# Optimization experiments

Measured on AMD Instinct MI355X. Metric: run time of the kernel, lower is better.

The kernel has to match this reference:

```python
import jax, jax.numpy as jnp
import numpy as np

B, M, H = 8, 2048, 1024


def setup_inputs() -> dict:
    key = jax.random.key(0)
    k0, k1, k2, k3, k4 = jax.random.split(key, 5)
    return {
        "query": jax.random.normal(k0, (B, M, H), dtype=jnp.float32),
        "key": jax.random.normal(k1, (B, M, H), dtype=jnp.float32),
        "span": jax.random.uniform(k2, (B, M, 2), dtype=jnp.float32),
        "value": jax.random.normal(k3, (B, M, H), dtype=jnp.float32),
        "key_pe": jax.random.normal(k4, (1, H, M), dtype=jnp.float32),
    }


def reference(query, key, span, value, key_pe):
    # Faithful to the source's returned value:
    #   attn_cont (span-gathered version) is overwritten by the dense q @ k^T,
    #   and the scaled/softmaxed `attn` (content + positional) is computed but
    #   NEVER used for the output. The module returns attn_cont @ value with
    #   no scaling and no softmax. span / key_pe do not affect the output.
    attn_cont = jnp.einsum('bmh,bnh->bmn', query, key)  # [B, M, M]
    out = jnp.matmul(attn_cont, value)                   # [B, M, H]
    return out
```

## Files before the change

kernel.cpp:

```cpp
#include <hip/hip_runtime.h>
#include <hip/hip_bf16.h>

typedef __attribute__((ext_vector_type(4))) float f32x4;
typedef __attribute__((ext_vector_type(8))) short bf16x8;
typedef __attribute__((ext_vector_type(2))) unsigned int u32x2;
typedef unsigned short u16;
typedef unsigned int u32;


__device__ __forceinline__ u16 f2bf(float f) {
  union { float f; unsigned int u; } v;
  v.f = f;
  unsigned int r = (v.u + 0x7fffu + ((v.u >> 16) & 1u)) >> 16;
  return (u16)r;
}

__device__ __forceinline__ u32 pk2(float a, float b) {
  u32 r;
  asm("v_cvt_pk_bf16_f32 %0, %1, %2" : "=v"(r) : "v"(a), "v"(b));
  return r;
}

__device__ __forceinline__ void async16(const void* g, const void* l) {
  __builtin_amdgcn_global_load_lds(
      (const __attribute__((address_space(1))) unsigned int*)(unsigned long)g,
      (__attribute__((address_space(3))) unsigned int*)(unsigned int)(unsigned long)l,
      16, 0, 0);
}

__device__ __forceinline__ void bar() {
  asm volatile("" ::: "memory");
  __builtin_amdgcn_s_barrier();
  asm volatile("" ::: "memory");
}

#define WAIT_LGKM0() asm volatile("s_waitcnt lgkmcnt(0)" ::: "memory")
#define WAIT_VM0()   asm volatile("s_waitcnt vmcnt(0)" ::: "memory")

#define G8(r) ((((r) >> 3) ^ (r)) & 7)

__global__ __launch_bounds__(512, 2) void gemmA(const float* __restrict__ V,
                                                const float* __restrict__ Kf,
                                                u16* __restrict__ Pt) {
  __shared__ u16 As[2][128][64];
  __shared__ u16 Bs[2][256][64];

  const int bid = blockIdx.x;
  const int b = bid & 7;
  const int tile = bid >> 3;
  const int bn0 = (tile & 3) * 256;
  const int bm0 = (tile >> 2) * 128;

  const int tid = threadIdx.x;
  const int lane = tid & 63;
  const int wave = tid >> 6;
  const int wr = wave >> 2;
  const int wc = wave & 3;
  const int l16 = lane & 15;
  const int kh = lane >> 4;

  const int dq = tid & 31, nq = tid >> 5;

  const char* pV = (const char*)(V + (long)b * 2048 * 1024 +
                                 (long)(nq * 4) * 1024 + bm0 + dq * 4);
  const char* pK = (const char*)(Kf + (long)b * 2048 * 1024 +
                                 (long)(nq * 4) * 1024 + bn0 + dq * 4);

  int awo[4], bwo[2][4];
#pragma unroll
  for (int j = 0; j < 4; ++j) {
    int r = dq * 4 + j;
    awo[j] = r * 128 + (((nq >> 1) ^ G8(r)) * 16) + (nq & 1) * 8;
  }
#pragma unroll
  for (int h = 0; h < 2; ++h)
#pragma unroll
    for (int j = 0; j < 4; ++j) {
      int r = h * 128 + dq * 4 + j;
      bwo[h][j] = r * 128 + (((nq >> 1) ^ G8(r)) * 16) + (nq & 1) * 8;
    }

  int offA[2][2][2], offB[2][2][2];
#pragma unroll
  for (int q = 0; q < 2; ++q)
#pragma unroll
    for (int f = 0; f < 2; ++f) {
      int rA = q * 64 + wr * 32 + f * 16 + l16;
      int rB = q * 128 + wc * 32 + f * 16 + l16;
#pragma unroll
      for (int ks = 0; ks < 2; ++ks) {
        offA[q][f][ks] = rA * 64 + (((ks * 4 + kh) ^ G8(rA)) * 8);
        offB[q][f][ks] = rB * 64 + (((ks * 4 + kh) ^ G8(rB)) * 8);
      }
    }

  f32x4 acc[4][4] = {};
  f32x4 aq[4], bq[8];
  bf16x8 ar[2][2], br[4][2];

#pragma unroll
  for (int j = 0; j < 4; ++j) aq[j] = *(const f32x4*)(pV + j * 4096);
#pragma unroll
  for (int h = 0; h < 2; ++h)
#pragma unroll
    for (int j = 0; j < 4; ++j)
      bq[h * 4 + j] = *(const f32x4*)(pK + h * 512 + j * 4096);
  pV += 262144; pK += 262144;
  {
    char* dA = (char*)&As[0][0][0];
    char* dB = (char*)&Bs[0][0][0];
#pragma unroll
    for (int j = 0; j < 4; ++j) {
      u32x2 v; v.x = pk2(aq[0][j], aq[1][j]); v.y = pk2(aq[2][j], aq[3][j]);
      *(u32x2*)(dA + awo[j]) = v;
    }
#pragma unroll
    for (int h = 0; h < 2; ++h)
#pragma unroll
      for (int j = 0; j < 4; ++j) {
        u32x2 v; v.x = pk2(bq[h * 4 + 0][j], bq[h * 4 + 1][j]);
        v.y = pk2(bq[h * 4 + 2][j], bq[h * 4 + 3][j]);
        *(u32x2*)(dB + bwo[h][j]) = v;
      }
  }
  WAIT_LGKM0();
  bar();

  const int NT = 32;
  for (int t = 0; t < NT; ++t) {
    const int cur = t & 1, nxt = cur ^ 1;
    const bool g = (t + 1 < NT);
    const u16* Ab = &As[cur][0][0];
    const u16* Bb = &Bs[cur][0][0];

#pragma unroll
    for (int f = 0; f < 2; ++f)
#pragma unroll
      for (int ks = 0; ks < 2; ++ks)
        ar[f][ks] = *(const bf16x8*)(Ab + offA[0][f][ks]);
#pragma unroll
    for (int q = 0; q < 2; ++q)
#pragma unroll
      for (int f = 0; f < 2; ++f)
#pragma unroll
        for (int ks = 0; ks < 2; ++ks)
          br[q * 2 + f][ks] = *(const bf16x8*)(Bb + offB[q][f][ks]);

    if (g) {
#pragma unroll
      for (int j = 0; j < 4; ++j) aq[j] = *(const f32x4*)(pV + j * 4096);
#pragma unroll
      for (int h = 0; h < 2; ++h)
#pragma unroll
        for (int j = 0; j < 4; ++j)
          bq[h * 4 + j] = *(const f32x4*)(pK + h * 512 + j * 4096);
      pV += 262144; pK += 262144;
    }

    __builtin_amdgcn_s_setprio(1);
#pragma unroll
    for (int f = 0; f < 2; ++f)
#pragma unroll
      for (int n = 0; n < 4; ++n)
#pragma unroll
        for (int ks = 0; ks < 2; ++ks)
          acc[f][n] = __builtin_amdgcn_mfma_f32_16x16x32_bf16(
              ar[f][ks], br[n][ks], acc[f][n], 0, 0, 0);
    __builtin_amdgcn_s_setprio(0);

#pragma unroll
    for (int f = 0; f < 2; ++f)
#pragma unroll
      for (int ks = 0; ks < 2; ++ks)
        ar[f][ks] = *(const bf16x8*)(Ab + offA[1][f][ks]);

    if (g) {
      char* dA = (char*)&As[nxt][0][0];
      char* dB = (char*)&Bs[nxt][0][0];
#pragma unroll
      for (int j = 0; j < 4; ++j) {
        u32x2 v; v.x = pk2(aq[0][j], aq[1][j]); v.y = pk2(aq[2][j], aq[3][j]);
        *(u32x2*)(dA + awo[j]) = v;
      }
#pragma unroll
      for (int h = 0; h < 2; ++h)
#pragma unroll
        for (int j = 0; j < 4; ++j) {
          u32x2 v; v.x = pk2(bq[h * 4 + 0][j], bq[h * 4 + 1][j]);
          v.y = pk2(bq[h * 4 + 2][j], bq[h * 4 + 3][j]);
          *(u32x2*)(dB + bwo[h][j]) = v;
        }
    }

    __builtin_amdgcn_s_setprio(1);
#pragma unroll
    for (int f = 0; f < 2; ++f)
#pragma unroll
      for (int n = 0; n < 4; ++n)
#pragma unroll
        for (int ks = 0; ks < 2; ++ks)
          acc[2 + f][n] = __builtin_amdgcn_mfma_f32_16x16x32_bf16(
              ar[f][ks], br[n][ks], acc[2 + f][n], 0, 0, 0);
    __builtin_amdgcn_s_setprio(0);

    WAIT_LGKM0();
    bar();
  }

  u16* Cb = Pt + (long)b * 1024 * 1024;
#pragma unroll
  for (int fm = 0; fm < 4; ++fm) {
    const int gm = bm0 + (fm >> 1) * 64 + wr * 32 + (fm & 1) * 16 + kh * 4;
#pragma unroll
    for (int fn = 0; fn < 4; ++fn) {
      const int gn = bn0 + (fn >> 1) * 128 + wc * 32 + (fn & 1) * 16 + l16;
#pragma unroll
      for (int r = 0; r < 4; ++r)
        Cb[(long)(gm + r) * 1024 + gn] = f2bf(acc[fm][fn][r]);
    }
  }
}

__global__ __launch_bounds__(512, 2) void gemmB(const float* __restrict__ Q,
                                                const u16* __restrict__ Pt,
                                                float* __restrict__ out) {
  __shared__ u16 As[2][256][64];
  __shared__ u16 Bs[2][2][128][64];

  const int bid = blockIdx.x;
  const int b = bid & 7;
  const int tile = bid >> 3;
  const int bn0 = (tile & 3) * 256;
  const int bm0 = (tile >> 2) * 256;

  const int tid = threadIdx.x;
  const int lane = tid & 63;
  const int wave = tid >> 6;
  const int wr = wave >> 2;
  const int wc = wave & 3;
  const int l16 = lane & 15;
  const int kh = lane >> 4;

  const int mrow = tid >> 4;
  const char* pQ = (const char*)(Q + (long)b * 2048 * 1024 +
                                 (long)(bm0 + mrow) * 1024 + (tid & 15) * 4);

  int qwo[8];
#pragma unroll
  for (int p = 0; p < 8; ++p) {
    int r = p * 32 + mrow;
    qwo[p] = r * 128 + ((((tid & 15) >> 1) ^ G8(r)) * 16) + (tid & 1) * 8;
  }

  int boff[2][2];
#pragma unroll
  for (int h = 0; h < 2; ++h)
#pragma unroll
    for (int i = 0; i < 2; ++i) {
      int u = tid + i * 512;
      int row = u >> 3, sl = (u & 7) ^ (row & 7);
      boff[h][i] = (bn0 + h * 128 + row) * 2048 + sl * 16;
    }
  const char* PtB = (const char*)(Pt + (long)b * 1024 * 1024);

  int offA[2][4][2];
#pragma unroll
  for (int q = 0; q < 2; ++q)
#pragma unroll
    for (int f = 0; f < 4; ++f) {
      int r = q * 128 + wr * 64 + f * 16 + l16;
#pragma unroll
      for (int ks = 0; ks < 2; ++ks)
        offA[q][f][ks] = r * 64 + (((ks * 4 + kh) ^ G8(r)) * 8);
    }
  int offBf[2][2];
#pragma unroll
  for (int g_ = 0; g_ < 2; ++g_) {
    int r = wc * 32 + g_ * 16 + l16;
#pragma unroll
    for (int ks = 0; ks < 2; ++ks)
      offBf[g_][ks] = r * 64 + (((ks * 4 + kh) ^ (l16 & 7)) * 8);
  }

#define STG_PT(h, buf)                                                      \
  {                                                                         \
    _Pragma("unroll") for (int i_ = 0; i_ < 2; ++i_) {                      \
      async16(PtB + boff[h][i_],                                            \
              (char*)&Bs[buf][h][0][0] + (tid + i_ * 512) * 16);            \
      boff[h][i_] += 128;                                                   \
    }                                                                       \
  }

  f32x4 acc[8][4] = {};
  f32x4 qv[8];
  bf16x8 ar[4][2], br[4][2];

#pragma unroll
  for (int p = 0; p < 8; ++p) qv[p] = *(const f32x4*)(pQ + p * 131072);
  STG_PT(0, 0);
  STG_PT(1, 0);
  {
    char* dA = (char*)&As[0][0][0];
#pragma unroll
    for (int p = 0; p < 8; ++p) {
      u32x2 v; v.x = pk2(qv[p].x, qv[p].y); v.y = pk2(qv[p].z, qv[p].w);
      *(u32x2*)(dA + qwo[p]) = v;
    }
  }
  pQ += 256;
  WAIT_VM0();
  WAIT_LGKM0();
  bar();

  const int NT = 16;
  for (int t = 0; t < NT; ++t) {
    const int cur = t & 1, nxt = cur ^ 1;
    const bool g = (t + 1 < NT);
    const u16* Ab = &As[cur][0][0];

#pragma unroll
    for (int f = 0; f < 4; ++f)
#pragma unroll
      for (int ks = 0; ks < 2; ++ks)
        ar[f][ks] = *(const bf16x8*)(Ab + offA[0][f][ks]);
#pragma unroll
    for (int qn = 0; qn < 2; ++qn)
#pragma unroll
      for (int g_ = 0; g_ < 2; ++g_)
#pragma unroll
        for (int ks = 0; ks < 2; ++ks)
          br[qn * 2 + g_][ks] =
              *(const bf16x8*)(&Bs[cur][qn][0][0] + offBf[g_][ks]);

    if (g) {
#pragma unroll
      for (int p = 0; p < 8; ++p) qv[p] = *(const f32x4*)(pQ + p * 131072);
      STG_PT(0, nxt);
      STG_PT(1, nxt);
    }

    __builtin_amdgcn_s_setprio(1);
#pragma unroll
    for (int f = 0; f < 4; ++f)
#pragma unroll
      for (int n = 0; n < 4; ++n)
#pragma unroll
        for (int ks = 0; ks < 2; ++ks)
          acc[f][n] = __builtin_amdgcn_mfma_f32_16x16x32_bf16(
              ar[f][ks], br[n][ks], acc[f][n], 0, 0, 0);
    __builtin_amdgcn_s_setprio(0);

#pragma unroll
    for (int f = 0; f < 4; ++f)
#pragma unroll
      for (int ks = 0; ks < 2; ++ks)
        ar[f][ks] = *(const bf16x8*)(Ab + offA[1][f][ks]);

    if (g) {
      char* dA = (char*)&As[nxt][0][0];
#pragma unroll
      for (int p = 0; p < 8; ++p) {
        u32x2 v; v.x = pk2(qv[p].x, qv[p].y); v.y = pk2(qv[p].z, qv[p].w);
        *(u32x2*)(dA + qwo[p]) = v;
      }
      pQ += 256;
    }

    __builtin_amdgcn_s_setprio(1);
#pragma unroll
    for (int f = 0; f < 4; ++f)
#pragma unroll
      for (int n = 0; n < 4; ++n)
#pragma unroll
        for (int ks = 0; ks < 2; ++ks)
          acc[4 + f][n] = __builtin_amdgcn_mfma_f32_16x16x32_bf16(
              ar[f][ks], br[n][ks], acc[4 + f][n], 0, 0, 0);
    __builtin_amdgcn_s_setprio(0);

    if (g) WAIT_VM0();
    WAIT_LGKM0();
    bar();
  }

  float* Cf = out + (long)b * 2048 * 1024;
#pragma unroll
  for (int fm = 0; fm < 8; ++fm) {
    const int gm = bm0 + (fm >> 2) * 128 + wr * 64 + (fm & 3) * 16 + kh * 4;
#pragma unroll
    for (int fn = 0; fn < 4; ++fn) {
      const int gn = bn0 + (fn >> 1) * 128 + wc * 32 + (fn & 1) * 16 + l16;
#pragma unroll
      for (int r = 0; r < 4; ++r)
        Cf[(long)(gm + r) * 1024 + gn] = acc[fm][fn][r];
    }
  }
#undef STG_PT
}


extern "C" void kernel_launch(void* const* d_in, const int* in_sizes, int n_in,
                              void* d_out, int out_size, void* d_ws, size_t ws_size,
                              hipStream_t stream) {
  const float* Q  = (const float*)d_in[0];
  const float* Kf = (const float*)d_in[1];
  const float* V  = (const float*)d_in[3];
  float* out = (float*)d_out;

  u16* Pt = (u16*)d_ws;

  gemmA<<<256, 512, 0, stream>>>(V, Kf, Pt);

  gemmB<<<256, 512, 0, stream>>>(Q, Pt, out);
}
```

Baseline: 130.8 us.

## Pre-convert K and V to transposed bf16, stream gemmA via async LDS loads

Adds a separate kernel that converts K and V from fp32 to bf16 and transposes them into workspace buffers, so the contraction dimension becomes contiguous. gemmA then loads its tiles with direct global-to-LDS async copies instead of fp32 register loads followed by pack-and-store, and its block tile changes from 128x256 to 256x128. The goal is to halve gemmA's global read bytes and remove the conversion and LDS write work from its main loop. In exchange it adds an extra launch plus a full read of K and V and a write of their bf16 copies, and it needs a larger workspace.

```diff
diff --git a/kernel.cpp b/kernel.cpp
--- a/kernel.cpp
+++ b/kernel.cpp
@@ -36,20 +36,54 @@
 
 #define WAIT_LGKM0() asm volatile("s_waitcnt lgkmcnt(0)" ::: "memory")
 #define WAIT_VM0()   asm volatile("s_waitcnt vmcnt(0)" ::: "memory")
-
 #define G8(r) ((((r) >> 3) ^ (r)) & 7)
 
-__global__ __launch_bounds__(512, 2) void gemmA(const float* __restrict__ V,
-                                                const float* __restrict__ Kf,
+
+__global__ __launch_bounds__(256) void cvt_kv(const float* __restrict__ Kin,
+                                              const float* __restrict__ Vin,
+                                              u16* __restrict__ Kt,
+                                              u16* __restrict__ Vt) {
+  __shared__ u16 tile[64][68];
+  const int z = blockIdx.z;
+  const int bsel = z >> 1;
+  const float* in = (z & 1) ? Kin : Vin;
+  u16* out = (z & 1) ? Kt : Vt;
+  const long bo = (long)bsel * 2048 * 1024;
+  const int r0 = blockIdx.y * 64;
+  const int c0 = blockIdx.x * 64;
+  const int t = threadIdx.x;
+  const int tr = t >> 4;
+  const int tc4 = (t & 15) * 4;
+
+#pragma unroll
+  for (int i = 0; i < 4; ++i) {
+    int r = i * 16 + tr;
+    f32x4 v = *(const f32x4*)(in + bo + (long)(r0 + r) * 1024 + c0 + tc4);
+    tile[tc4 + 0][r] = f2bf(v.x);
+    tile[tc4 + 1][r] = f2bf(v.y);
+    tile[tc4 + 2][r] = f2bf(v.z);
+    tile[tc4 + 3][r] = f2bf(v.w);
+  }
+  __syncthreads();
+#pragma unroll
+  for (int i = 0; i < 4; ++i) {
+    int c = i * 16 + tr;
+    ushort4 u = *(const ushort4*)(&tile[c][tc4]);
+    *(ushort4*)(out + bo + (long)(c0 + c) * 2048 + r0 + tc4) = u;
+  }
+}
+
+__global__ __launch_bounds__(512, 2) void gemmA(const u16* __restrict__ Vt,
+                                                const u16* __restrict__ Kt,
                                                 u16* __restrict__ Pt) {
-  __shared__ u16 As[2][128][64];
-  __shared__ u16 Bs[2][256][64];
+  __shared__ u16 As[2][256][64];
+  __shared__ u16 Bs[2][128][64];
 
   const int bid = blockIdx.x;
   const int b = bid & 7;
   const int tile = bid >> 3;
-  const int bn0 = (tile & 3) * 256;
-  const int bm0 = (tile >> 2) * 128;
+  const int bn0 = (tile & 7) * 128;
+  const int bm0 = (tile >> 3) * 256;
 
   const int tid = threadIdx.x;
   const int lane = tid & 63;
@@ -59,109 +93,89 @@
   const int l16 = lane & 15;
   const int kh = lane >> 4;
 
-  const int dq = tid & 31, nq = tid >> 5;
-
-  const char* pV = (const char*)(V + (long)b * 2048 * 1024 +
-                                 (long)(nq * 4) * 1024 + bm0 + dq * 4);
-  const char* pK = (const char*)(Kf + (long)b * 2048 * 1024 +
-                                 (long)(nq * 4) * 1024 + bn0 + dq * 4);
-
-  int awo[4], bwo[2][4];
-#pragma unroll
-  for (int j = 0; j < 4; ++j) {
-    int r = dq * 4 + j;
-    awo[j] = r * 128 + (((nq >> 1) ^ G8(r)) * 16) + (nq & 1) * 8;
-  }
-#pragma unroll
-  for (int h = 0; h < 2; ++h)
-#pragma unroll
-    for (int j = 0; j < 4; ++j) {
-      int r = h * 128 + dq * 4 + j;
-      bwo[h][j] = r * 128 + (((nq >> 1) ^ G8(r)) * 16) + (nq & 1) * 8;
-    }
-
-  int offA[2][2][2], offB[2][2][2];
+  const char* Ab = (const char*)(Vt + (long)b * 1024 * 2048);
+  const char* Bb = (const char*)(Kt + (long)b * 1024 * 2048);
+
+  int aoff[4], boff[2];
+#pragma unroll
+  for (int i = 0; i < 4; ++i) {
+    int u = tid + i * 512;
+    int row = u >> 3, sl = (u & 7) ^ (row & 7);
+    aoff[i] = (bm0 + row) * 4096 + sl * 16;
+  }
+#pragma unroll
+  for (int i = 0; i < 2; ++i) {
+    int u = tid + i * 512;
+    int row = u >> 3, sl = (u & 7) ^ (row & 7);
+    boff[i] = (bn0 + row) * 4096 + sl * 16;
+  }
+
+#define STG_A(buf)                                                          \
+  {                                                                         \
+    _Pragma("unroll") for (int i_ = 0; i_ < 4; ++i_) {                      \
+      async16(Ab + aoff[i_], (char*)&As[buf][0][0] + (tid + i_ * 512) * 16);\
+      aoff[i_] += 128;                                                      \
+    }                                                                       \
+  }
+#define STG_B(buf)                                                          \
+  {                                                                         \
+    _Pragma("unroll") for (int i_ = 0; i_ < 2; ++i_) {                      \
+      async16(Bb + boff[i_], (char*)&Bs[buf][0][0] + (tid + i_ * 512) * 16);\
+      boff[i_] += 128;                                                      \
+    }                                                                       \
+  }
+
+  int offA[2][4][2];
 #pragma unroll
   for (int q = 0; q < 2; ++q)
 #pragma unroll
-    for (int f = 0; f < 2; ++f) {
-      int rA = q * 64 + wr * 32 + f * 16 + l16;
-      int rB = q * 128 + wc * 32 + f * 16 + l16;
-#pragma unroll
-      for (int ks = 0; ks < 2; ++ks) {
-        offA[q][f][ks] = rA * 64 + (((ks * 4 + kh) ^ G8(rA)) * 8);
-        offB[q][f][ks] = rB * 64 + (((ks * 4 + kh) ^ G8(rB)) * 8);
-      }
-    }
-
-  f32x4 acc[4][4] = {};
-  f32x4 aq[4], bq[8];
-  bf16x8 ar[2][2], br[4][2];
-
-#pragma unroll
-  for (int j = 0; j < 4; ++j) aq[j] = *(const f32x4*)(pV + j * 4096);
-#pragma unroll
-  for (int h = 0; h < 2; ++h)
-#pragma unroll
-    for (int j = 0; j < 4; ++j)
-      bq[h * 4 + j] = *(const f32x4*)(pK + h * 512 + j * 4096);
-  pV += 262144; pK += 262144;
-  {
-    char* dA = (char*)&As[0][0][0];
-    char* dB = (char*)&Bs[0][0][0];
-#pragma unroll
-    for (int j = 0; j < 4; ++j) {
-      u32x2 v; v.x = pk2(aq[0][j], aq[1][j]); v.y = pk2(aq[2][j], aq[3][j]);
-      *(u32x2*)(dA + awo[j]) = v;
-    }
-#pragma unroll
-    for (int h = 0; h < 2; ++h)
-#pragma unroll
-      for (int j = 0; j < 4; ++j) {
-        u32x2 v; v.x = pk2(bq[h * 4 + 0][j], bq[h * 4 + 1][j]);
-        v.y = pk2(bq[h * 4 + 2][j], bq[h * 4 + 3][j]);
-        *(u32x2*)(dB + bwo[h][j]) = v;
-      }
-  }
-  WAIT_LGKM0();
+    for (int f = 0; f < 4; ++f) {
+      int r = q * 128 + wr * 64 + f * 16 + l16;
+#pragma unroll
+      for (int ks = 0; ks < 2; ++ks)
+        offA[q][f][ks] = r * 64 + (((ks * 4 + kh) ^ (l16 & 7)) * 8);
+    }
+  int offB[2][2];
+#pragma unroll
+  for (int fn = 0; fn < 2; ++fn) {
+    int r = fn * 64 + wc * 16 + l16;
+#pragma unroll
+    for (int ks = 0; ks < 2; ++ks)
+      offB[fn][ks] = r * 64 + (((ks * 4 + kh) ^ (l16 & 7)) * 8);
+  }
+
+  f32x4 acc[8][2] = {};
+  bf16x8 ar[4][2], br[2][2];
+
+  STG_A(0); STG_B(0);
+  WAIT_VM0();
   bar();
 
   const int NT = 32;
   for (int t = 0; t < NT; ++t) {
     const int cur = t & 1, nxt = cur ^ 1;
     const bool g = (t + 1 < NT);
-    const u16* Ab = &As[cur][0][0];
-    const u16* Bb = &Bs[cur][0][0];
-
-#pragma unroll
-    for (int f = 0; f < 2; ++f)
-#pragma unroll
-      for (int ks = 0; ks < 2; ++ks)
-        ar[f][ks] = *(const bf16x8*)(Ab + offA[0][f][ks]);
-#pragma unroll
-    for (int q = 0; q < 2; ++q)
-#pragma unroll
-      for (int f = 0; f < 2; ++f)
-#pragma unroll
-        for (int ks = 0; ks < 2; ++ks)
-          br[q * 2 + f][ks] = *(const bf16x8*)(Bb + offB[q][f][ks]);
-
-    if (g) {
-#pragma unroll
-      for (int j = 0; j < 4; ++j) aq[j] = *(const f32x4*)(pV + j * 4096);
-#pragma unroll
-      for (int h = 0; h < 2; ++h)
-#pragma unroll
-        for (int j = 0; j < 4; ++j)
-          bq[h * 4 + j] = *(const f32x4*)(pK + h * 512 + j * 4096);
-      pV += 262144; pK += 262144;
-    }
+    const u16* Abuf = &As[cur][0][0];
+    const u16* Bbuf = &Bs[cur][0][0];
+
+#pragma unroll
+    for (int f = 0; f < 4; ++f)
+#pragma unroll
+      for (int ks = 0; ks < 2; ++ks)
+        ar[f][ks] = *(const bf16x8*)(Abuf + offA[0][f][ks]);
+#pragma unroll
+    for (int fn = 0; fn < 2; ++fn)
+#pragma unroll
+      for (int ks = 0; ks < 2; ++ks)
+        br[fn][ks] = *(const bf16x8*)(Bbuf + offB[fn][ks]);
+
+    if (g) { STG_A(nxt); STG_B(nxt); }
 
     __builtin_amdgcn_s_setprio(1);
 #pragma unroll
-    for (int f = 0; f < 2; ++f)
-#pragma unroll
-      for (int n = 0; n < 4; ++n)
+    for (int f = 0; f < 4; ++f)
+#pragma unroll
+      for (int n = 0; n < 2; ++n)
 #pragma unroll
         for (int ks = 0; ks < 2; ++ks)
           acc[f][n] = __builtin_amdgcn_mfma_f32_16x16x32_bf16(
@@ -169,51 +183,35 @@
     __builtin_amdgcn_s_setprio(0);
 
 #pragma unroll
-    for (int f = 0; f < 2; ++f)
-#pragma unroll
-      for (int ks = 0; ks < 2; ++ks)
-        ar[f][ks] = *(const bf16x8*)(Ab + offA[1][f][ks]);
-
-    if (g) {
-      char* dA = (char*)&As[nxt][0][0];
-      char* dB = (char*)&Bs[nxt][0][0];
-#pragma unroll
-      for (int j = 0; j < 4; ++j) {
-        u32x2 v; v.x = pk2(aq[0][j], aq[1][j]); v.y = pk2(aq[2][j], aq[3][j]);
-        *(u32x2*)(dA + awo[j]) = v;
-      }
-#pragma unroll
-      for (int h = 0; h < 2; ++h)
-#pragma unroll
-        for (int j = 0; j < 4; ++j) {
-          u32x2 v; v.x = pk2(bq[h * 4 + 0][j], bq[h * 4 + 1][j]);
-          v.y = pk2(bq[h * 4 + 2][j], bq[h * 4 + 3][j]);
-          *(u32x2*)(dB + bwo[h][j]) = v;
-        }
-    }
+    for (int f = 0; f < 4; ++f)
+#pragma unroll
+      for (int ks = 0; ks < 2; ++ks)
+        ar[f][ks] = *(const bf16x8*)(Abuf + offA[1][f][ks]);
 
     __builtin_amdgcn_s_setprio(1);
 #pragma unroll
-    for (int f = 0; f < 2; ++f)
-#pragma unroll
-      for (int n = 0; n < 4; ++n)
+    for (int f = 0; f < 4; ++f)
+#pragma unroll
+      for (int n = 0; n < 2; ++n)
 #pragma unroll
         for (int ks = 0; ks < 2; ++ks)
-          acc[2 + f][n] = __builtin_amdgcn_mfma_f32_16x16x32_bf16(
-              ar[f][ks], br[n][ks], acc[2 + f][n], 0, 0, 0);
+          acc[4 + f][n] = __builtin_amdgcn_mfma_f32_16x16x32_bf16(
+              ar[f][ks], br[n][ks], acc[4 + f][n], 0, 0, 0);
     __builtin_amdgcn_s_setprio(0);
 
-    WAIT_LGKM0();
+    if (g) WAIT_VM0();
     bar();
   }
+#undef STG_A
+#undef STG_B
 
   u16* Cb = Pt + (long)b * 1024 * 1024;
 #pragma unroll
-  for (int fm = 0; fm < 4; ++fm) {
-    const int gm = bm0 + (fm >> 1) * 64 + wr * 32 + (fm & 1) * 16 + kh * 4;
-#pragma unroll
-    for (int fn = 0; fn < 4; ++fn) {
-      const int gn = bn0 + (fn >> 1) * 128 + wc * 32 + (fn & 1) * 16 + l16;
+  for (int fm = 0; fm < 8; ++fm) {
+    const int gm = bm0 + (fm >> 2) * 128 + wr * 64 + (fm & 3) * 16 + kh * 4;
+#pragma unroll
+    for (int fn = 0; fn < 2; ++fn) {
+      const int gn = bn0 + fn * 64 + wc * 16 + l16;
 #pragma unroll
       for (int r = 0; r < 4; ++r)
         Cb[(long)(gm + r) * 1024 + gn] = f2bf(acc[fm][fn][r]);
@@ -406,9 +404,14 @@
   const float* V  = (const float*)d_in[3];
   float* out = (float*)d_out;
 
-  u16* Pt = (u16*)d_ws;
-
-  gemmA<<<256, 512, 0, stream>>>(V, Kf, Pt);
+  char* ws = (char*)d_ws;
+  u16* Vt = (u16*)(ws);
+  u16* Kt = (u16*)(ws + (size_t)32 * 1024 * 1024);
+  u16* Pt = (u16*)(ws + (size_t)64 * 1024 * 1024);
+
+  cvt_kv<<<dim3(16, 32, 16), 256, 0, stream>>>(Kf, V, Kt, Vt);
+
+  gemmA<<<256, 512, 0, stream>>>(Vt, Kt, Pt);
 
   gemmB<<<256, 512, 0, stream>>>(Q, Pt, out);
 }
```

Measured after the change: 134.9 us. 3.1% more time.
